# Kernel optimization log

Measured on AMD Instinct MI355X. Metric: run time of the kernel, lower is better.

The kernel has to match this reference:

```python
import jax, jax.numpy as jnp
import numpy as np

TOP_K = 2
CAPACITY_FACTOR = 1.25
LOAD_BALANCE_WEIGHT = 0.01
ROUTER_Z_WEIGHT = 0.001


def setup_inputs() -> dict:
    key = jax.random.key(0)
    k1, k2, k3, k4, k5 = jax.random.split(key, 5)
    B, S, D, F, E = 4, 2048, 1024, 4096, 8
    x = jax.random.normal(k1, (B, S, D), dtype=jnp.float32)
    gate_w = jax.random.normal(k2, (E, D), dtype=jnp.float32) * 0.02
    wi_gate = jax.random.normal(k3, (E, F, D), dtype=jnp.float32) * 0.02
    wi_up = jax.random.normal(k4, (E, F, D), dtype=jnp.float32) * 0.02
    wo = jax.random.normal(k5, (E, D, F), dtype=jnp.float32) * 0.02
    return {"x": x, "gate_w": gate_w, "wi_gate": wi_gate, "wi_up": wi_up, "wo": wo}


def _dispatch_combine_one_k(x_flat, eids, ew, wi_gate, wi_up, wo, capacity):
    """Capacity-limited dispatch (first-come positions), GeGLU expert, combine."""
    N, D = x_flat.shape
    E = wi_gate.shape[0]
    # position of each token within its expert's queue (count of earlier tokens
    # assigned to the same expert) -- matches the atomic counter semantics in order.
    oh = jax.nn.one_hot(eids, E, dtype=jnp.int32)            # [N, E]
    pos = jnp.cumsum(oh, axis=0) - oh                        # counts strictly before
    pos = jnp.take_along_axis(pos, eids[:, None], axis=1)[:, 0]  # [N]
    valid = pos < capacity
    pos_safe = jnp.where(valid, pos, capacity)               # overflow bucket
    # dispatched_x[e, c, :] = x of the token at slot (e, c); zeros where empty
    disp = jnp.zeros((E, capacity + 1, D), x_flat.dtype).at[eids, pos_safe].set(x_flat)
    disp = disp[:, :capacity]                                # drop overflow bucket
    # grouped GeGLU expert: batched GEMMs over experts
    gate_h = jax.nn.silu(jnp.einsum('ecd,efd->ecf', disp, wi_gate))
    up_h = jnp.einsum('ecd,efd->ecf', disp, wi_up)
    eout = jnp.einsum('ecf,edf->ecd', gate_h * up_h, wo)     # [E, cap, D]
    # combine: gather each token's expert output, weight, zero dropped tokens
    y = eout[eids, jnp.minimum(pos, capacity - 1)]           # [N, D]
    return y * (ew * valid.astype(x_flat.dtype))[:, None]


def reference(x, gate_w, wi_gate, wi_up, wo):
    B, S, D = x.shape
    E = gate_w.shape[0]
    N = B * S
    capacity = max(int(N / E * CAPACITY_FACTOR), 1)
    x_flat = x.reshape(N, D)
    router_logits = x_flat @ gate_w.T                        # [N, E]
    router_probs = jax.nn.softmax(router_logits, axis=-1)
    topk_probs, topk_idx = jax.lax.top_k(router_probs, TOP_K)
    topk_probs = topk_probs / jnp.sum(topk_probs, axis=-1, keepdims=True)
    out = jnp.zeros_like(x_flat)
    for k in range(TOP_K):
        out = out + _dispatch_combine_one_k(
            x_flat, topk_idx[:, k], topk_probs[:, k], wi_gate, wi_up, wo, capacity)
    # aux losses: Switch-style load balance + router z-loss
    density = jnp.mean(jax.nn.one_hot(topk_idx, E, dtype=x.dtype).sum(axis=1), axis=0) / TOP_K
    mean_probs = jnp.mean(router_probs, axis=0)
    lb_loss = LOAD_BALANCE_WEIGHT * E * jnp.sum(density * mean_probs)
    z_loss = ROUTER_Z_WEIGHT * jnp.mean(jax.scipy.special.logsumexp(router_logits, axis=-1) ** 2)
    aux_loss = lb_loss + z_loss
    return out.reshape(B, S, D), aux_loss
```

## Files before the change

### kernel.cpp

```cpp
#include <hip/hip_runtime.h>
#include <cstdint>
#include <cstddef>

#define N_TOK 8192
#define DDIM  1024
#define FDIM  4096
#define NEXP  8
#define CAP   1280
#define MPE   2560
#define NSLOT (NEXP * MPE)

typedef __attribute__((ext_vector_type(8))) __bf16 bf16x8;
typedef __attribute__((ext_vector_type(4))) float  f32x4;

__device__ __forceinline__ unsigned short f2bf(float f) {
    unsigned int u = __float_as_uint(f);
    u += 0x7fffu + ((u >> 16) & 1u);
    return (unsigned short)(u >> 16);
}
__device__ __forceinline__ float bf2f(unsigned short s) {
    return __uint_as_float(((unsigned int)s) << 16);
}

__device__ __forceinline__ void async_cp16(const void* g, void* l) {
    __builtin_amdgcn_global_load_lds(
        (const __attribute__((address_space(1))) unsigned int*)g,
        (__attribute__((address_space(3))) unsigned int*)l, 16, 0, 0);
}

__global__ __launch_bounds__(256) void convert_wi_kernel(
    const float* __restrict__ wi_gate, const float* __restrict__ wi_up,
    unsigned short* __restrict__ wcomb)
{
    const int idx = blockIdx.x * 256 + threadIdx.x;
    const int d8 = idx & 127;
    const int r  = (idx >> 7) & 8191;
    const int e  = idx >> 20;
    const int f  = (r >> 7) * 64 + (r & 63);
    const float* src = (((r >> 6) & 1) ? wi_up : wi_gate)
                       + ((size_t)(e * FDIM + f) * DDIM + d8 * 8);
    const float4 a = ((const float4*)src)[0];
    const float4 b = ((const float4*)src)[1];
    uint4 o;
    o.x = (unsigned)f2bf(a.x) | ((unsigned)f2bf(a.y) << 16);
    o.y = (unsigned)f2bf(a.z) | ((unsigned)f2bf(a.w) << 16);
    o.z = (unsigned)f2bf(b.x) | ((unsigned)f2bf(b.y) << 16);
    o.w = (unsigned)f2bf(b.z) | ((unsigned)f2bf(b.w) << 16);
    *(uint4*)(wcomb + (size_t)idx * 8) = o;
}

__global__ __launch_bounds__(256) void convert_wo_kernel(
    const float* __restrict__ wo, unsigned short* __restrict__ wo_bf)
{
    const int idx = blockIdx.x * 256 + threadIdx.x;
    const float4 a = ((const float4*)(wo + (size_t)idx * 8))[0];
    const float4 b = ((const float4*)(wo + (size_t)idx * 8))[1];
    uint4 o;
    o.x = (unsigned)f2bf(a.x) | ((unsigned)f2bf(a.y) << 16);
    o.y = (unsigned)f2bf(a.z) | ((unsigned)f2bf(a.w) << 16);
    o.z = (unsigned)f2bf(b.x) | ((unsigned)f2bf(b.y) << 16);
    o.w = (unsigned)f2bf(b.z) | ((unsigned)f2bf(b.w) << 16);
    *(uint4*)(wo_bf + (size_t)idx * 8) = o;
}

__global__ __launch_bounds__(256) void router_kernel(
    const float* __restrict__ x, const float* __restrict__ gate_w,
    int* __restrict__ topk_idx, float* __restrict__ topk_w,
    float* __restrict__ stats)
{
    const int wave = threadIdx.x >> 6, lane = threadIdx.x & 63;
    const int n = blockIdx.x * 4 + wave;
    const float4* xp = (const float4*)(x + (size_t)n * DDIM + lane * 16);
    float4 xv[4];
#pragma unroll
    for (int i = 0; i < 4; i++) xv[i] = xp[i];
    float part[NEXP];
#pragma unroll
    for (int e = 0; e < NEXP; e++) {
        const float4* gp = (const float4*)(gate_w + (size_t)e * DDIM + lane * 16);
        float s = 0.f;
#pragma unroll
        for (int i = 0; i < 4; i++) {
            const float4 g = gp[i];
            s += xv[i].x * g.x + xv[i].y * g.y + xv[i].z * g.z + xv[i].w * g.w;
        }
        part[e] = s;
    }
#pragma unroll
    for (int off = 32; off > 0; off >>= 1)
#pragma unroll
        for (int e = 0; e < NEXP; e++) part[e] += __shfl_down(part[e], off);
    if (lane == 0) {
        float p[NEXP];
        float m = -1e30f;
#pragma unroll
        for (int e = 0; e < NEXP; e++) m = fmaxf(m, part[e]);
        float sum = 0.f;
#pragma unroll
        for (int e = 0; e < NEXP; e++) { p[e] = __expf(part[e] - m); sum += p[e]; }
        const float inv = 1.f / sum;
#pragma unroll
        for (int e = 0; e < NEXP; e++) p[e] *= inv;
        const float lse = m + __logf(sum);
        int e1 = 0; float p1 = p[0];
#pragma unroll
        for (int e = 1; e < NEXP; e++) if (p[e] > p1) { p1 = p[e]; e1 = e; }
        int e2 = -1; float p2 = -1.f;
#pragma unroll
        for (int e = 0; e < NEXP; e++) if (e != e1 && p[e] > p2) { p2 = p[e]; e2 = e; }
        const float wsum = p1 + p2;
        topk_idx[n * 2 + 0] = e1; topk_idx[n * 2 + 1] = e2;
        topk_w[n * 2 + 0] = p1 / wsum; topk_w[n * 2 + 1] = p2 / wsum;
        float* sp = stats + (n & 63) * 17;
#pragma unroll
        for (int e = 0; e < NEXP; e++) atomicAdd(sp + e, p[e]);
        atomicAdd(sp + 8 + e1, 1.f);
        atomicAdd(sp + 8 + e2, 1.f);
        atomicAdd(sp + 16, lse * lse);
    }
}

__global__ __launch_bounds__(512) void pos_kernel(
    const int* __restrict__ topk_idx, const float* __restrict__ topk_w,
    int* __restrict__ slot_tok, int* __restrict__ tok2slot, int* __restrict__ gcnt)
{
    __shared__ int cnt[2][NEXP][256];
    const int t = threadIdx.x;
    for (int i = t; i < NSLOT; i += 512) slot_tok[i] = -1;
    const int kk = t >> 8;
    const int c  = t & 255;
    int lc[NEXP];
#pragma unroll
    for (int e = 0; e < NEXP; e++) lc[e] = 0;
    const int base_n = c * 32;
    for (int i = 0; i < 32; i++) lc[topk_idx[(base_n + i) * 2 + kk]]++;
#pragma unroll
    for (int e = 0; e < NEXP; e++) cnt[kk][e][c] = lc[e];
    __syncthreads();
    if (t < 16) {
        const int k2 = t >> 3, e = t & 7;
        int run = 0;
        for (int c2 = 0; c2 < 256; c2++) { int v = cnt[k2][e][c2]; cnt[k2][e][c2] = run; run += v; }
        gcnt[e * 2 + k2] = run < CAP ? run : CAP;
    }
    __syncthreads();
    int run[NEXP];
#pragma unroll
    for (int e = 0; e < NEXP; e++) run[e] = cnt[kk][e][c];
    for (int i = 0; i < 32; i++) {
        const int n = base_n + i;
        const int e = topk_idx[n * 2 + kk];
        const int p = run[e]++;
        if (p < CAP) {
            const int slot = (e * 2 + kk) * CAP + p;
            slot_tok[slot] = n;
            tok2slot[n * 2 + kk] = slot;
        } else {
            tok2slot[n * 2 + kk] = -1;
        }
    }
}

__global__ __launch_bounds__(128) void dispatch_kernel(
    const float* __restrict__ x, const int* __restrict__ slot_tok,
    unsigned short* __restrict__ disp)
{
    const int slot = blockIdx.x;
    const int t = threadIdx.x;
    const int token = slot_tok[slot];
    uint4 o = make_uint4(0u, 0u, 0u, 0u);
    if (token >= 0) {
        const float4* src = (const float4*)(x + (size_t)token * DDIM + t * 8);
        const float4 a = src[0];
        const float4 b = src[1];
        o.x = (unsigned)f2bf(a.x) | ((unsigned)f2bf(a.y) << 16);
        o.y = (unsigned)f2bf(a.z) | ((unsigned)f2bf(a.w) << 16);
        o.z = (unsigned)f2bf(b.x) | ((unsigned)f2bf(b.y) << 16);
        o.w = (unsigned)f2bf(b.z) | ((unsigned)f2bf(b.w) << 16);
    }
    *(uint4*)(disp + (size_t)slot * DDIM + t * 8) = o;
}

template<int KDIM, int BROWS, int NT, int EPI>
__global__ __launch_bounds__(512, 2) void gemm256(
    const unsigned short* __restrict__ A,
    const unsigned short* __restrict__ Bw,
    const int* __restrict__ gcnt,
    unsigned short* __restrict__ outp)
{
    constexpr int NKT = KDIM / 32;
    __shared__ __align__(16) unsigned short smem[65536];
    const int b = blockIdx.x;
    const int e    = b / (2 * 5 * NT);
    const int rem  = b % (2 * 5 * NT);
    const int kk   = rem / (5 * NT);
    const int rem2 = rem % (5 * NT);
    const int mt = rem2 / NT, nt = rem2 % NT;
    if (mt * 256 >= gcnt[e * 2 + kk]) return;

    const int t = threadIdx.x;
    const int wave = t >> 6, lane = t & 63;
    const unsigned short* Asrc = A  + (size_t)(e * MPE + kk * CAP + mt * 256) * KDIM;
    const unsigned short* Bsrc = Bw + ((size_t)e * BROWS + (size_t)nt * 256) * KDIM;

    const int srow = t >> 2;
    const int qg   = (((t & 3) ^ ((srow >> 1) & 3)) * 8);
    const size_t soff0 = (size_t)srow * KDIM + qg;
    const size_t soff1 = (size_t)(srow + 128) * KDIM + qg;
    const int lb0 = wave * 512, lb1 = 4096 + wave * 512;

#define STG(c, kt) do { \
        const size_t ko_ = (size_t)(kt) * 32; \
        async_cp16(Asrc + soff0 + ko_, &smem[(c) * 16384 + lb0]); \
        async_cp16(Asrc + soff1 + ko_, &smem[(c) * 16384 + lb1]); \
        async_cp16(Bsrc + soff0 + ko_, &smem[(c) * 16384 + 8192 + lb0]); \
        async_cp16(Bsrc + soff1 + ko_, &smem[(c) * 16384 + 8192 + lb1]); } while (0)

    const int wm = wave >> 2, wn = wave & 3;
    const int lrow = lane & 15, lk = lane >> 4;
    const int lkx = (lk ^ ((lrow >> 1) & 3)) * 8;
    const int aro = (wm * 128 + lrow) * 32 + lkx;
    const int bro = 8192 + (wn * 64 + lrow) * 32 + lkx;

    const f32x4 fzero = {0.f, 0.f, 0.f, 0.f};
    f32x4 acc[8][4];
#pragma unroll
    for (int i = 0; i < 8; i++)
#pragma unroll
        for (int j = 0; j < 4; j++) acc[i][j] = fzero;

#define RD(SA, SB, c) do { \
        _Pragma("unroll") for (int i_ = 0; i_ < 8; i_++) \
            SA[i_] = *(const bf16x8*)&smem[(c) * 16384 + aro + i_ * 512]; \
        _Pragma("unroll") for (int j_ = 0; j_ < 4; j_++) \
            SB[j_] = *(const bf16x8*)&smem[(c) * 16384 + bro + j_ * 512]; } while (0)

#define MM(SA, SB) do { \
        __builtin_amdgcn_s_setprio(1); \
        _Pragma("unroll") for (int i_ = 0; i_ < 8; i_++) \
            _Pragma("unroll") for (int j_ = 0; j_ < 4; j_++) \
                acc[i_][j_] = __builtin_amdgcn_mfma_f32_16x16x32_bf16(SA[i_], SB[j_], acc[i_][j_], 0, 0, 0); \
        __builtin_amdgcn_s_setprio(0); } while (0)

#define BODY(kt, CA, CB, NA, NB) do { \
        if ((kt) < NKT - 2) asm volatile("s_waitcnt vmcnt(4)" ::: "memory"); \
        else                asm volatile("s_waitcnt vmcnt(0)" ::: "memory"); \
        __builtin_amdgcn_s_barrier(); \
        if ((kt) + 1 < NKT) RD(NA, NB, ((kt) + 1) & 3); \
        if ((kt) + 3 < NKT) STG(((kt) + 3) & 3, (kt) + 3); \
        __builtin_amdgcn_sched_barrier(0); \
        MM(CA, CB); } while (0)

    STG(0, 0); STG(1, 1); STG(2, 2);
    asm volatile("s_waitcnt vmcnt(8)" ::: "memory");
    __builtin_amdgcn_s_barrier();

    bf16x8 afA[8], bfA[4], afB[8], bfB[4];
    RD(afA, bfA, 0);

#pragma unroll 1
    for (int m = 0; m < NKT / 2; m++) {
        BODY(2 * m,     afA, bfA, afB, bfB);
        BODY(2 * m + 1, afB, bfB, afA, bfA);
    }
#undef BODY
#undef MM
#undef RD
#undef STG

    if constexpr (EPI == 1) {
        __syncthreads();
        const int g = wn >> 1;
        const int epb = g * 17408;
        if ((wn & 1) == 0) {
#pragma unroll
            for (int i = 0; i < 8; i++)
#pragma unroll
                for (int j = 0; j < 4; j++)
#pragma unroll
                    for (int r = 0; r < 4; r++)
                        smem[epb + (wm * 128 + i * 16 + lk * 4 + r) * 68 + j * 16 + lrow] = f2bf(acc[i][j][r]);
        }
        __syncthreads();
        if (wn & 1) {
#pragma unroll
            for (int i = 0; i < 8; i++)
#pragma unroll
                for (int r = 0; r < 4; r++) {
                    const int mrow = wm * 128 + i * 16 + lk * 4 + r;
                    const size_t base = (size_t)(e * MPE + kk * CAP + mt * 256 + mrow) * FDIM + (nt * 2 + g) * 64;
#pragma unroll
                    for (int j = 0; j < 4; j++) {
                        const float gv = bf2f(smem[epb + mrow * 68 + j * 16 + lrow]);
                        const float u  = acc[i][j][r];
                        const float a  = (gv / (1.f + __expf(-gv))) * u;
                        outp[base + j * 16 + lrow] = f2bf(a);
                    }
                }
        }
    } else {
#pragma unroll
        for (int i = 0; i < 8; i++)
#pragma unroll
            for (int r = 0; r < 4; r++) {
                const int orow = e * MPE + kk * CAP + mt * 256 + wm * 128 + i * 16 + lk * 4 + r;
                const size_t obase = (size_t)orow * DDIM + nt * 256 + wn * 64;
#pragma unroll
                for (int j = 0; j < 4; j++)
                    outp[obase + j * 16 + lrow] = f2bf(acc[i][j][r]);
            }
    }
}

__global__ __launch_bounds__(256) void combine_kernel(
    const unsigned short* __restrict__ eout,
    const int* __restrict__ tok2slot, const float* __restrict__ topk_w,
    float* __restrict__ out)
{
    const int n = blockIdx.x;
    const int t = threadIdx.x;
    const int s0 = tok2slot[n * 2 + 0], s1 = tok2slot[n * 2 + 1];
    const float w0 = (s0 >= 0) ? topk_w[n * 2 + 0] : 0.f;
    const float w1 = (s1 >= 0) ? topk_w[n * 2 + 1] : 0.f;
    const int a0 = (s0 >= 0) ? s0 : 0;
    const int a1 = (s1 >= 0) ? s1 : 0;
    const uint2 p0 = *(const uint2*)(eout + (size_t)a0 * DDIM + t * 4);
    const uint2 p1 = *(const uint2*)(eout + (size_t)a1 * DDIM + t * 4);
    float4 o;
    o.x = w0 * bf2f((unsigned short)(p0.x & 0xffff)) + w1 * bf2f((unsigned short)(p1.x & 0xffff));
    o.y = w0 * bf2f((unsigned short)(p0.x >> 16))    + w1 * bf2f((unsigned short)(p1.x >> 16));
    o.z = w0 * bf2f((unsigned short)(p0.y & 0xffff)) + w1 * bf2f((unsigned short)(p1.y & 0xffff));
    o.w = w0 * bf2f((unsigned short)(p0.y >> 16))    + w1 * bf2f((unsigned short)(p1.y >> 16));
    *(float4*)(out + (size_t)n * DDIM + t * 4) = o;
}

__global__ void aux_kernel(const float* __restrict__ stats, float* __restrict__ out)
{
    if (threadIdx.x == 0 && blockIdx.x == 0) {
        float ps[NEXP], cn[NEXP], z = 0.f;
#pragma unroll
        for (int e = 0; e < NEXP; e++) { ps[e] = 0.f; cn[e] = 0.f; }
        for (int c = 0; c < 64; c++) {
            const float* sp = stats + c * 17;
#pragma unroll
            for (int e = 0; e < NEXP; e++) { ps[e] += sp[e]; cn[e] += sp[8 + e]; }
            z += sp[16];
        }
        float lb = 0.f;
#pragma unroll
        for (int e = 0; e < NEXP; e++)
            lb += (cn[e] / (2.f * N_TOK)) * (ps[e] / N_TOK);
        const float aux = 0.01f * 8.f * lb + 0.001f * (z / N_TOK);
        out[(size_t)N_TOK * DDIM] = aux;
    }
}

extern "C" void kernel_launch(void* const* d_in, const int* in_sizes, int n_in,
                              void* d_out, int out_size, void* d_ws, size_t ws_size,
                              hipStream_t stream)
{
    (void)in_sizes; (void)n_in; (void)ws_size; (void)out_size;
    const float* x       = (const float*)d_in[0];
    const float* gate_w  = (const float*)d_in[1];
    const float* wi_gate = (const float*)d_in[2];
    const float* wi_up   = (const float*)d_in[3];
    const float* wo      = (const float*)d_in[4];
    float* out = (float*)d_out;
    char* ws = (char*)d_ws;

    int*            topk_idx = (int*)(ws + 0);
    float*          topk_w   = (float*)(ws + 65536);
    int*            slot_tok = (int*)(ws + 131072);
    int*            tok2slot = (int*)(ws + 212992);
    float*          stats    = (float*)(ws + 278528);
    int*            gcnt     = (int*)(ws + 282880);
    unsigned short* disp     = (unsigned short*)(ws + 524288);
    unsigned short* act      = (unsigned short*)(ws + 42467328);
    unsigned short* eout     = (unsigned short*)(ws + 210239488);
    unsigned short* wcomb    = (unsigned short*)(ws + 252182528);
    unsigned short* wo_bf    = (unsigned short*)(ws + 386400256);

    hipMemsetAsync(stats, 0, 64 * 17 * sizeof(float), stream);

    convert_wi_kernel<<<32768, 256, 0, stream>>>(wi_gate, wi_up, wcomb);
    convert_wo_kernel<<<16384, 256, 0, stream>>>(wo, wo_bf);
    router_kernel<<<N_TOK / 4, 256, 0, stream>>>(x, gate_w, topk_idx, topk_w, stats);
    pos_kernel<<<1, 512, 0, stream>>>(topk_idx, topk_w, slot_tok, tok2slot, gcnt);
    dispatch_kernel<<<NSLOT, 128, 0, stream>>>(x, slot_tok, disp);
    gemm256<1024, 8192, 32, 1><<<NEXP * 2 * 5 * 32, 512, 0, stream>>>(disp, wcomb, gcnt, act);
    gemm256<4096, 1024, 4, 0><<<NEXP * 2 * 5 * 4, 512, 0, stream>>>(act, wo_bf, gcnt, eout);
    combine_kernel<<<N_TOK, 256, 0, stream>>>(eout, tok2slot, topk_w, out);
    aux_kernel<<<1, 64, 0, stream>>>(stats, out);
}
```

Baseline: 1.101 ms.

## Restructure GEMM main loop to 64-wide K tiles with 4-phase staggered prefetch

Each GEMM K tile grows from 32 to 64, with a matching 8-way XOR swizzle, and the 4-stage ring buffer becomes a 2-buffer scheme. Each K step is split into four MFMA sub-phases that interleave LDS reads and half-tile async global loads, with A and B prefetched at different distances. The aim is finer-grained overlap of memory and MFMA work and half as many loop iterations. In exchange it adds more barriers per tile and shallower prefetch depth, and the buffer reuse timing is delicate.

```diff
diff --git a/kernel.cpp b/kernel.cpp
--- a/kernel.cpp
+++ b/kernel.cpp
@@ -188,7 +188,7 @@
     const int* __restrict__ gcnt,
     unsigned short* __restrict__ outp)
 {
-    constexpr int NKT = KDIM / 32;
+    constexpr int NKT = KDIM / 64;
     __shared__ __align__(16) unsigned short smem[65536];
     const int b = blockIdx.x;
     const int e    = b / (2 * 5 * NT);
@@ -203,25 +203,27 @@
     const unsigned short* Asrc = A  + (size_t)(e * MPE + kk * CAP + mt * 256) * KDIM;
     const unsigned short* Bsrc = Bw + ((size_t)e * BROWS + (size_t)nt * 256) * KDIM;
 
-    const int srow = t >> 2;
-    const int qg   = (((t & 3) ^ ((srow >> 1) & 3)) * 8);
-    const size_t soff0 = (size_t)srow * KDIM + qg;
-    const size_t soff1 = (size_t)(srow + 128) * KDIM + qg;
-    const int lb0 = wave * 512, lb1 = 4096 + wave * 512;
-
-#define STG(c, kt) do { \
-        const size_t ko_ = (size_t)(kt) * 32; \
-        async_cp16(Asrc + soff0 + ko_, &smem[(c) * 16384 + lb0]); \
-        async_cp16(Asrc + soff1 + ko_, &smem[(c) * 16384 + lb1]); \
-        async_cp16(Bsrc + soff0 + ko_, &smem[(c) * 16384 + 8192 + lb0]); \
-        async_cp16(Bsrc + soff1 + ko_, &smem[(c) * 16384 + 8192 + lb1]); } while (0)
+    const int rl = t >> 3;
+    const int q  = t & 7;
+    const int qx = (q ^ ((rl >> 1) & 7)) * 8;
+    const size_t sbase = (size_t)rl * KDIM + qx;
+    const int dbase = wave * 512;
+
+#define STG_H(c, mat, h, kt) do { \
+        const unsigned short* s_ = ((mat) ? Bsrc : Asrc) + (size_t)(h) * 128 * KDIM + (size_t)(kt) * 64 + sbase; \
+        unsigned short* d_ = &smem[(c) * 32768 + (mat) * 16384 + (h) * 8192 + dbase]; \
+        async_cp16(s_, d_); \
+        async_cp16(s_ + (size_t)64 * KDIM, d_ + 4096); } while (0)
 
     const int wm = wave >> 2, wn = wave & 3;
     const int lrow = lane & 15, lk = lane >> 4;
-    const int lkx = (lk ^ ((lrow >> 1) & 3)) * 8;
-    const int aro = (wm * 128 + lrow) * 32 + lkx;
-    const int bro = 8192 + (wn * 64 + lrow) * 32 + lkx;
-
+    const int xr   = (lrow >> 1) & 7;
+    const int aoff = (wm * 128 + lrow) * 64;
+    const int boff = 16384 + (wn * 64 + lrow) * 64;
+    const int k0x = ((0 + lk) ^ xr) * 8;
+    const int k1x = ((4 + lk) ^ xr) * 8;
+
+    bf16x8 a[4][2], bf[4][2];
     const f32x4 fzero = {0.f, 0.f, 0.f, 0.f};
     f32x4 acc[8][4];
 #pragma unroll
@@ -229,44 +231,68 @@
 #pragma unroll
         for (int j = 0; j < 4; j++) acc[i][j] = fzero;
 
-#define RD(SA, SB, c) do { \
-        _Pragma("unroll") for (int i_ = 0; i_ < 8; i_++) \
-            SA[i_] = *(const bf16x8*)&smem[(c) * 16384 + aro + i_ * 512]; \
-        _Pragma("unroll") for (int j_ = 0; j_ < 4; j_++) \
-            SB[j_] = *(const bf16x8*)&smem[(c) * 16384 + bro + j_ * 512]; } while (0)
-
-#define MM(SA, SB) do { \
-        __builtin_amdgcn_s_setprio(1); \
-        _Pragma("unroll") for (int i_ = 0; i_ < 8; i_++) \
-            _Pragma("unroll") for (int j_ = 0; j_ < 4; j_++) \
-                acc[i_][j_] = __builtin_amdgcn_mfma_f32_16x16x32_bf16(SA[i_], SB[j_], acc[i_][j_], 0, 0, 0); \
-        __builtin_amdgcn_s_setprio(0); } while (0)
-
-#define BODY(kt, CA, CB, NA, NB) do { \
-        if ((kt) < NKT - 2) asm volatile("s_waitcnt vmcnt(4)" ::: "memory"); \
+#define RD_A(c, ib) do { \
+        _Pragma("unroll") for (int i_ = 0; i_ < 4; i_++) { \
+            a[i_][0] = *(const bf16x8*)&smem[(c) * 32768 + aoff + ((ib) + i_) * 1024 + k0x]; \
+            a[i_][1] = *(const bf16x8*)&smem[(c) * 32768 + aoff + ((ib) + i_) * 1024 + k1x]; } } while (0)
+#define RD_B(c, jb) do { \
+        _Pragma("unroll") for (int j_ = 0; j_ < 2; j_++) { \
+            bf[(jb) + j_][0] = *(const bf16x8*)&smem[(c) * 32768 + boff + ((jb) + j_) * 1024 + k0x]; \
+            bf[(jb) + j_][1] = *(const bf16x8*)&smem[(c) * 32768 + boff + ((jb) + j_) * 1024 + k1x]; } } while (0)
+#define MM16(ib, jb) do { \
+        _Pragma("unroll") for (int ks_ = 0; ks_ < 2; ks_++) \
+        _Pragma("unroll") for (int i_ = 0; i_ < 4; i_++) \
+        _Pragma("unroll") for (int j_ = 0; j_ < 2; j_++) \
+            acc[(ib) + i_][(jb) + j_] = __builtin_amdgcn_mfma_f32_16x16x32_bf16( \
+                a[i_][ks_], bf[(jb) + j_][ks_], acc[(ib) + i_][(jb) + j_], 0, 0, 0); } while (0)
+
+#define PH_TOP() do { \
+        __builtin_amdgcn_s_barrier(); \
+        asm volatile("s_waitcnt lgkmcnt(0)" ::: "memory"); \
+        __builtin_amdgcn_sched_barrier(0); \
+        __builtin_amdgcn_s_setprio(1); } while (0)
+#define PH_BOT() do { \
+        __builtin_amdgcn_s_setprio(0); \
+        __builtin_amdgcn_s_barrier(); } while (0)
+
+#define KT_BODY(kt, c) do { \
+         \
+        RD_A(c, 0); RD_B(c, 0); \
+        if ((kt) + 1 < NKT) STG_H((c) ^ 1, 0, 0, (kt) + 1); \
+        PH_TOP(); MM16(0, 0); PH_BOT(); \
+         \
+        RD_B(c, 2); \
+        if ((kt) + 1 < NKT) STG_H((c) ^ 1, 0, 1, (kt) + 1); \
+        PH_TOP(); MM16(0, 2); PH_BOT(); \
+         \
+        RD_A(c, 4); \
+        if ((kt) + 2 < NKT) STG_H(c, 1, 0, (kt) + 2); \
+        PH_TOP(); MM16(4, 0); PH_BOT(); \
+         \
+        if ((kt) + 2 < NKT) STG_H(c, 1, 1, (kt) + 2); \
+        PH_TOP(); MM16(4, 2); \
+        __builtin_amdgcn_s_setprio(0); \
+        if ((kt) + 2 < NKT) asm volatile("s_waitcnt vmcnt(4)" ::: "memory"); \
         else                asm volatile("s_waitcnt vmcnt(0)" ::: "memory"); \
-        __builtin_amdgcn_s_barrier(); \
-        if ((kt) + 1 < NKT) RD(NA, NB, ((kt) + 1) & 3); \
-        if ((kt) + 3 < NKT) STG(((kt) + 3) & 3, (kt) + 3); \
-        __builtin_amdgcn_sched_barrier(0); \
-        MM(CA, CB); } while (0)
-
-    STG(0, 0); STG(1, 1); STG(2, 2);
-    asm volatile("s_waitcnt vmcnt(8)" ::: "memory");
+        __builtin_amdgcn_s_barrier(); } while (0)
+
+    STG_H(0, 0, 0, 0); STG_H(0, 0, 1, 0); STG_H(0, 1, 0, 0); STG_H(0, 1, 1, 0);
+    STG_H(1, 1, 0, 1); STG_H(1, 1, 1, 1);
+    asm volatile("s_waitcnt vmcnt(4)" ::: "memory");
     __builtin_amdgcn_s_barrier();
 
-    bf16x8 afA[8], bfA[4], afB[8], bfB[4];
-    RD(afA, bfA, 0);
-
 #pragma unroll 1
-    for (int m = 0; m < NKT / 2; m++) {
-        BODY(2 * m,     afA, bfA, afB, bfB);
-        BODY(2 * m + 1, afB, bfB, afA, bfA);
-    }
-#undef BODY
-#undef MM
-#undef RD
-#undef STG
+    for (int m2 = 0; m2 < NKT / 2; ++m2) {
+        KT_BODY(2 * m2, 0);
+        KT_BODY(2 * m2 + 1, 1);
+    }
+#undef KT_BODY
+#undef PH_TOP
+#undef PH_BOT
+#undef MM16
+#undef RD_A
+#undef RD_B
+#undef STG_H
 
     if constexpr (EPI == 1) {
         __syncthreads();
@@ -293,8 +319,8 @@
                     for (int j = 0; j < 4; j++) {
                         const float gv = bf2f(smem[epb + mrow * 68 + j * 16 + lrow]);
                         const float u  = acc[i][j][r];
-                        const float a  = (gv / (1.f + __expf(-gv))) * u;
-                        outp[base + j * 16 + lrow] = f2bf(a);
+                        const float aa = (gv / (1.f + __expf(-gv))) * u;
+                        outp[base + j * 16 + lrow] = f2bf(aa);
                     }
                 }
         }
```

Measured after the change: 1.050 ms. -4.7%, faster.
